# Optimization experiments

Hardware: AMD Instinct MI355X
Metric: run time of the kernel (lower is better)

The kernel has to match this reference:

```python
import jax, jax.numpy as jnp
import numpy as np

B, L, IN_DIM, H, DK, DV = 4, 512, 256, 8, 32, 32
TEMP = DK ** 0.5  # temperature = d_k ** 0.5
LN_EPS = 1e-6


def setup_inputs() -> dict:
    key = jax.random.key(0)
    ks = jax.random.split(key, 5)
    s = 0.05
    return {
        "x": jax.random.normal(ks[0], (B, L, IN_DIM), jnp.float32),
        "w_q": jax.random.normal(ks[1], (IN_DIM, H * DK), jnp.float32) * s,
        "w_k": jax.random.normal(ks[2], (IN_DIM, H * DK), jnp.float32) * s,
        "w_v": jax.random.normal(ks[3], (IN_DIM, H * DV), jnp.float32) * s,
        "w_fc": jax.random.normal(ks[4], (H * DV, IN_DIM), jnp.float32) * s,
        "ln_gamma": jnp.ones((IN_DIM,), jnp.float32),
        "ln_beta": jnp.zeros((IN_DIM,), jnp.float32),
    }


def reference(x, w_q, w_k, w_v, w_fc, ln_gamma, ln_beta):
    # LayerNorm (biased variance, eps inside sqrt, as in torch.nn.LayerNorm)
    mu = jnp.mean(x, axis=-1, keepdims=True)
    var = jnp.var(x, axis=-1, keepdims=True)
    xn = (x - mu) / jnp.sqrt(var + LN_EPS) * ln_gamma + ln_beta
    residual = xn

    # Projections; torch layout after transpose(1,3) is [B, d, H, L]; per-head slice is [B, d, L].
    # We use [B, H, d, L] which yields identical per-head tensors (vectorized over heads).
    q = (xn @ w_q).reshape(B, L, H, DK).transpose(0, 2, 3, 1) / TEMP  # [B,H,DK,L]
    k = (xn @ w_k).reshape(B, L, H, DK).transpose(0, 2, 3, 1)          # [B,H,DK,L]
    v = (xn @ w_v).reshape(B, L, H, DV).transpose(0, 2, 3, 1)          # [B,H,DV,L]

    # L1 distance scores (note the source's index convention):
    # attn[b,h,i,j] = mean_d |q[b,h,d,j] - k[b,h,d,i]|   -> [B,H,L,L]
    attn = jnp.mean(jnp.abs(q[:, :, :, None, :] - k[:, :, :, :, None]), axis=2)
    attn = jax.nn.softmax(attn, axis=-1)

    # out[b,h,d,i] = sum_j v[b,h,d,j] * attn[b,h,i,j]   (torch: bmm(v, attn^T))
    out = jnp.einsum('bhdj,bhij->bhdi', v, attn)  # [B,H,DV,L]
    out = out.reshape(B, H * DV, L).transpose(0, 2, 1)  # head-major concat -> [B,L,H*DV]
    out = out @ w_fc + residual  # use_gamma=False path; dropout is identity at eval

    # extract_attn_map (no_grad in source)
    am = jax.lax.stop_gradient(attn)
    am = jnp.mean(am, axis=1)          # mean over heads -> [B,L,L]
    am = jnp.sum(am, axis=1)           # sum over key axis -> [B,L]
    mn = jnp.min(am, axis=1, keepdims=True)
    mx = jnp.max(am, axis=1, keepdims=True)
    am = (am - mn) / (mx - mn)
    return out, am
```

## Files before the change

kernel.cpp:

```cpp
#include <hip/hip_runtime.h>
#include <hip/hip_fp16.h>
#include <math.h>

#define BATCH 4
#define SEQ   512
#define IND   256
#define NH    8
#define DKV   32
#define BH    32
#define NTOK  2048

__device__ __forceinline__ __half2 habs2_(__half2 x) {
    unsigned u = __builtin_bit_cast(unsigned, x) & 0x7fff7fffu;
    return __builtin_bit_cast(__half2, u);
}
__device__ __forceinline__ __half2 shfl_xor_h2(__half2 x, int m) {
    float f = __builtin_bit_cast(float, x);
    f = __shfl_xor(f, m, 64);
    return __builtin_bit_cast(__half2, f);
}

__global__ void ln_kernel(const float* __restrict__ x,
                          const float* __restrict__ gamma,
                          const float* __restrict__ beta,
                          float* __restrict__ xn,
                          float* __restrict__ am) {
    int row = blockIdx.x;
    int t = threadIdx.x;
    if (blockIdx.x < 8) am[blockIdx.x * 256 + t] = 0.0f;
    float v = x[row * IND + t];
    float s = v, s2 = v * v;
    #pragma unroll
    for (int o = 32; o > 0; o >>= 1) {
        s  += __shfl_xor(s,  o, 64);
        s2 += __shfl_xor(s2, o, 64);
    }
    __shared__ float ls[4], ls2[4];
    int w = t >> 6;
    if ((t & 63) == 0) { ls[w] = s; ls2[w] = s2; }
    __syncthreads();
    s  = ls[0] + ls[1] + ls[2] + ls[3];
    s2 = ls2[0] + ls2[1] + ls2[2] + ls2[3];
    float mu  = s * (1.0f / IND);
    float var = s2 * (1.0f / IND) - mu * mu;
    float r = rsqrtf(var + 1e-6f);
    xn[row * IND + t] = (v - mu) * r * gamma[t] + beta[t];
}

__device__ __forceinline__ void gemm_tile_64(const float* __restrict__ A,
                                             const float* __restrict__ B,
                                             int m0, int n0, int ldb,
                                             float acc[4][4]) {
    __shared__ __align__(16) float As[2][32][68];
    __shared__ __align__(16) float Bs[2][32][68];
    const int t  = threadIdx.x;
    const int tx = t & 15, ty = t >> 4;
    const int am = t >> 3, ac = (t & 7) * 4;
    const int bk = t >> 4, bn = (t & 15) * 4;

    float4 a0, a1, b0, b1;
    auto loadG = [&](int kc) {
        a0 = *(const float4*)&A[(m0 + am) * IND + kc * 32 + ac];
        a1 = *(const float4*)&A[(m0 + 32 + am) * IND + kc * 32 + ac];
        b0 = *(const float4*)&B[(kc * 32 + bk) * ldb + n0 + bn];
        b1 = *(const float4*)&B[(kc * 32 + 16 + bk) * ldb + n0 + bn];
    };
    auto storeL = [&](int buf) {
        As[buf][ac + 0][am] = a0.x; As[buf][ac + 1][am] = a0.y;
        As[buf][ac + 2][am] = a0.z; As[buf][ac + 3][am] = a0.w;
        As[buf][ac + 0][am + 32] = a1.x; As[buf][ac + 1][am + 32] = a1.y;
        As[buf][ac + 2][am + 32] = a1.z; As[buf][ac + 3][am + 32] = a1.w;
        *(float4*)&Bs[buf][bk][bn]      = b0;
        *(float4*)&Bs[buf][16 + bk][bn] = b1;
    };

    loadG(0); storeL(0);
    for (int kc = 0; kc < 8; kc++) {
        __syncthreads();
        if (kc < 7) loadG(kc + 1);
        const int buf = kc & 1;
        #pragma unroll
        for (int kk = 0; kk < 32; kk++) {
            float4 av = *(const float4*)&As[buf][kk][ty * 4];
            float4 bv = *(const float4*)&Bs[buf][kk][tx * 4];
            acc[0][0] = fmaf(av.x, bv.x, acc[0][0]);
            acc[0][1] = fmaf(av.x, bv.y, acc[0][1]);
            acc[0][2] = fmaf(av.x, bv.z, acc[0][2]);
            acc[0][3] = fmaf(av.x, bv.w, acc[0][3]);
            acc[1][0] = fmaf(av.y, bv.x, acc[1][0]);
            acc[1][1] = fmaf(av.y, bv.y, acc[1][1]);
            acc[1][2] = fmaf(av.y, bv.z, acc[1][2]);
            acc[1][3] = fmaf(av.y, bv.w, acc[1][3]);
            acc[2][0] = fmaf(av.z, bv.x, acc[2][0]);
            acc[2][1] = fmaf(av.z, bv.y, acc[2][1]);
            acc[2][2] = fmaf(av.z, bv.z, acc[2][2]);
            acc[2][3] = fmaf(av.z, bv.w, acc[2][3]);
            acc[3][0] = fmaf(av.w, bv.x, acc[3][0]);
            acc[3][1] = fmaf(av.w, bv.y, acc[3][1]);
            acc[3][2] = fmaf(av.w, bv.z, acc[3][2]);
            acc[3][3] = fmaf(av.w, bv.w, acc[3][3]);
        }
        if (kc < 7) { __syncthreads(); storeL((kc + 1) & 1); }
    }
}

__global__ __launch_bounds__(256) void proj_kernel(
        const float* __restrict__ xn,
        const float* __restrict__ wq, const float* __restrict__ wk,
        const float* __restrict__ wv,
        __half* __restrict__ Q, __half* __restrict__ K, __half* __restrict__ V) {
    int which = blockIdx.z;
    const float* W = (which == 0) ? wq : (which == 1) ? wk : wv;
    __half* O = (which == 0) ? Q : (which == 1) ? K : V;
    int m0 = blockIdx.x * 64, n0 = blockIdx.y * 64;
    float acc[4][4] = {};
    gemm_tile_64(xn, W, m0, n0, IND, acc);
    float scale = (which == 0) ? 0.17677669529663687f : 1.0f;
    int tx = threadIdx.x & 15, ty = threadIdx.x >> 4;
    int col = n0 + tx * 4;
    int h = col >> 5, d = col & 31;
    #pragma unroll
    for (int r = 0; r < 4; r++) {
        int tok = m0 + ty * 4 + r;
        int b = tok >> 9, l = tok & 511;
        __half2 p0 = __halves2half2(__float2half_rn(acc[r][0] * scale),
                                    __float2half_rn(acc[r][1] * scale));
        __half2 p1 = __halves2half2(__float2half_rn(acc[r][2] * scale),
                                    __float2half_rn(acc[r][3] * scale));
        __half* dst = O + (((b << 3) + h) * SEQ + l) * DKV + d;
        *(__half2*)dst = p0;
        *(__half2*)(dst + 2) = p1;
    }
}

__global__ __launch_bounds__(256) void attn_kernel(
        const __half* __restrict__ Qh, const __half* __restrict__ Kh,
        const __half* __restrict__ Vh, float* __restrict__ attn_out,
        float* __restrict__ am) {
    __shared__ __align__(16) __half Th[2][128][40];
    const int t = threadIdx.x;
    const int gy = blockIdx.y;
    const int i0 = blockIdx.x * 16;
    const int b = gy >> 3, h = gy & 7;
    const __half* Qb = Qh + gy * SEQ * DKV;
    const __half* Kb = Kh + gy * SEQ * DKV;
    const __half* Vb = Vh + gy * SEQ * DKV;
    const int g = t >> 5, jl = t & 31;
    const int r0 = t >> 2, ch = t & 3;

    __half2 ka[16], kb[16];
    {
        const float4* pa = (const float4*)(Kb + (i0 + g) * DKV);
        const float4* pb = (const float4*)(Kb + (i0 + g + 8) * DKV);
        #pragma unroll
        for (int c = 0; c < 4; c++) {
            float4 va = pa[c], vb = pb[c];
            const __half2* ha = (const __half2*)&va;
            const __half2* hb = (const __half2*)&vb;
            #pragma unroll
            for (int k = 0; k < 4; k++) { ka[c*4+k] = ha[k]; kb[c*4+k] = hb[k]; }
        }
    }

    float vals_a[16], vals_b[16];
    float4 pre0, pre1;

    pre0 = *(const float4*)(Qb + r0 * DKV + ch * 8);
    pre1 = *(const float4*)(Qb + (r0 + 64) * DKV + ch * 8);
    *(float4*)&Th[0][r0][ch * 8] = pre0;
    *(float4*)&Th[0][r0 + 64][ch * 8] = pre1;
    __syncthreads();
    #pragma unroll
    for (int tile = 0; tile < 4; tile++) {
        const int buf = tile & 1;
        if (tile < 3) {
            pre0 = *(const float4*)(Qb + ((tile+1)*128 + r0) * DKV + ch * 8);
            pre1 = *(const float4*)(Qb + ((tile+1)*128 + r0 + 64) * DKV + ch * 8);
        }
        #pragma unroll
        for (int m = 0; m < 4; m++) {
            const int j = jl + m * 32;
            __half2 z = __float2half2_rn(0.0f);
            __half2 sa0 = z, sa1 = z, sb0 = z, sb1 = z;
            #pragma unroll
            for (int c = 0; c < 4; c++) {
                float4 qv = *(const float4*)&Th[buf][j][c * 8];
                const __half2* q2 = (const __half2*)&qv;
                #pragma unroll
                for (int k = 0; k < 4; k++) {
                    __half2 da = habs2_(__hsub2(q2[k], ka[c*4+k]));
                    __half2 db = habs2_(__hsub2(q2[k], kb[c*4+k]));
                    if (k & 1) { sa1 = __hadd2(sa1, da); sb1 = __hadd2(sb1, db); }
                    else       { sa0 = __hadd2(sa0, da); sb0 = __hadd2(sb0, db); }
                }
            }
            __half2 sa = __hadd2(sa0, sa1), sb = __hadd2(sb0, sb1);
            vals_a[tile*4+m] = (__low2float(sa) + __high2float(sa)) * (1.0f/32.0f);
            vals_b[tile*4+m] = (__low2float(sb) + __high2float(sb)) * (1.0f/32.0f);
        }
        if (tile < 3) {
            *(float4*)&Th[buf ^ 1][r0][ch * 8] = pre0;
            *(float4*)&Th[buf ^ 1][r0 + 64][ch * 8] = pre1;
        }
        __syncthreads();
    }

    float mxa = vals_a[0], mxb = vals_b[0];
    #pragma unroll
    for (int m = 1; m < 16; m++) {
        mxa = fmaxf(mxa, vals_a[m]); mxb = fmaxf(mxb, vals_b[m]);
    }
    #pragma unroll
    for (int s = 1; s <= 16; s <<= 1) {
        mxa = fmaxf(mxa, __shfl_xor(mxa, s, 64));
        mxb = fmaxf(mxb, __shfl_xor(mxb, s, 64));
    }
    float sua = 0.0f, sub = 0.0f;
    #pragma unroll
    for (int m = 0; m < 16; m++) {
        vals_a[m] = __expf(vals_a[m] - mxa); sua += vals_a[m];
        vals_b[m] = __expf(vals_b[m] - mxb); sub += vals_b[m];
    }
    #pragma unroll
    for (int s = 1; s <= 16; s <<= 1) {
        sua += __shfl_xor(sua, s, 64);
        sub += __shfl_xor(sub, s, 64);
    }
    float inva = 1.0f / sua, invb = 1.0f / sub;
    #pragma unroll
    for (int m = 0; m < 16; m++) { vals_a[m] *= inva; vals_b[m] *= invb; }

    __half2 acc_a[16], acc_b[16];
    #pragma unroll
    for (int k = 0; k < 16; k++) {
        acc_a[k] = __float2half2_rn(0.0f);
        acc_b[k] = __float2half2_rn(0.0f);
    }
    pre0 = *(const float4*)(Vb + r0 * DKV + ch * 8);
    pre1 = *(const float4*)(Vb + (r0 + 64) * DKV + ch * 8);
    *(float4*)&Th[0][r0][ch * 8] = pre0;
    *(float4*)&Th[0][r0 + 64][ch * 8] = pre1;
    __syncthreads();
    #pragma unroll
    for (int tile = 0; tile < 4; tile++) {
        const int buf = tile & 1;
        if (tile < 3) {
            pre0 = *(const float4*)(Vb + ((tile+1)*128 + r0) * DKV + ch * 8);
            pre1 = *(const float4*)(Vb + ((tile+1)*128 + r0 + 64) * DKV + ch * 8);
        }
        #pragma unroll
        for (int m = 0; m < 4; m++) {
            const int j = jl + m * 32;
            __half2 pa = __float2half2_rn(vals_a[tile*4+m]);
            __half2 pb = __float2half2_rn(vals_b[tile*4+m]);
            #pragma unroll
            for (int c = 0; c < 4; c++) {
                float4 vv = *(const float4*)&Th[buf][j][c * 8];
                const __half2* v2 = (const __half2*)&vv;
                #pragma unroll
                for (int k = 0; k < 4; k++) {
                    acc_a[c*4+k] = __hfma2(pa, v2[k], acc_a[c*4+k]);
                    acc_b[c*4+k] = __hfma2(pb, v2[k], acc_b[c*4+k]);
                }
            }
        }
        if (tile < 3) {
            *(float4*)&Th[buf ^ 1][r0][ch * 8] = pre0;
            *(float4*)&Th[buf ^ 1][r0 + 64][ch * 8] = pre1;
        }
        __syncthreads();
    }

#define REDSTEP(S, C)                                                      \
    {                                                                      \
        _Pragma("unroll")                                                  \
        for (int k = 0; k < (C); k++) {                                    \
            __half2 sa = (jl & (S)) ? acc_a[k] : acc_a[k + (C)];           \
            __half2 sb = (jl & (S)) ? acc_b[k] : acc_b[k + (C)];           \
            __half2 ra = shfl_xor_h2(sa, (S));                             \
            __half2 rb = shfl_xor_h2(sb, (S));                             \
            __half2 qa = (jl & (S)) ? acc_a[k + (C)] : acc_a[k];           \
            __half2 qb = (jl & (S)) ? acc_b[k + (C)] : acc_b[k];           \
            acc_a[k] = __hadd2(qa, ra);                                    \
            acc_b[k] = __hadd2(qb, rb);                                    \
        }                                                                  \
    }
    REDSTEP(16, 8)
    REDSTEP(8, 4)
    REDSTEP(4, 2)
    REDSTEP(2, 1)
#undef REDSTEP
    acc_a[0] = __hadd2(acc_a[0], shfl_xor_h2(acc_a[0], 1));
    acc_b[0] = __hadd2(acc_b[0], shfl_xor_h2(acc_b[0], 1));
    if (!(jl & 1)) {
        int d2 = (jl >> 1) & 15;
        int col = h * 32 + d2 * 2;
        float2 oa = make_float2(__low2float(acc_a[0]), __high2float(acc_a[0]));
        float2 ob = make_float2(__low2float(acc_b[0]), __high2float(acc_b[0]));
        *(float2*)&attn_out[(b * SEQ + i0 + g) * IND + col] = oa;
        *(float2*)&attn_out[(b * SEQ + i0 + g + 8) * IND + col] = ob;
    }

    float colp[16];
    #pragma unroll
    for (int m = 0; m < 16; m++) {
        float cp = vals_a[m] + vals_b[m];
        cp += __shfl_xor(cp, 32, 64);
        colp[m] = cp;
    }
    float* amw = (float*)&Th[0][0][0];
    const int w = t >> 6;
    if (!(t & 32)) {
        #pragma unroll
        for (int m = 0; m < 16; m++) {
            int j = (m >> 2) * 128 + (m & 3) * 32 + jl;
            amw[w * 512 + j] = colp[m];
        }
    }
    __syncthreads();
    #pragma unroll
    for (int n = 0; n < 2; n++) {
        int j = t + n * 256;
        float s = (amw[j] + amw[512 + j] + amw[1024 + j] + amw[1536 + j]) * 0.125f;
        atomicAdd(&am[b * SEQ + j], s);
    }
}

__global__ __launch_bounds__(256) void fc_kernel(
        const float* __restrict__ ao, const float* __restrict__ wfc,
        const float* __restrict__ xn, float* __restrict__ out) {
    int m0 = blockIdx.x * 64, n0 = blockIdx.y * 64;
    float acc[4][4] = {};
    gemm_tile_64(ao, wfc, m0, n0, IND, acc);
    int tx = threadIdx.x & 15, ty = threadIdx.x >> 4;
    #pragma unroll
    for (int r = 0; r < 4; r++) {
        int row = m0 + ty * 4 + r;
        float4 xr = *(const float4*)&xn[row * IND + n0 + tx * 4];
        float4 o = make_float4(acc[r][0] + xr.x, acc[r][1] + xr.y,
                               acc[r][2] + xr.z, acc[r][3] + xr.w);
        *(float4*)&out[row * IND + n0 + tx * 4] = o;
    }
}

__global__ void amnorm_kernel(const float* __restrict__ am,
                              float* __restrict__ out_am) {
    int b = blockIdx.x;
    int t = threadIdx.x;
    float v0 = am[b * SEQ + t];
    float v1 = am[b * SEQ + t + 256];
    float mn = fminf(v0, v1), mx = fmaxf(v0, v1);
    #pragma unroll
    for (int o = 32; o > 0; o >>= 1) {
        mn = fminf(mn, __shfl_xor(mn, o, 64));
        mx = fmaxf(mx, __shfl_xor(mx, o, 64));
    }
    __shared__ float lmn[4], lmx[4];
    int w = t >> 6;
    if ((t & 63) == 0) { lmn[w] = mn; lmx[w] = mx; }
    __syncthreads();
    mn = fminf(fminf(lmn[0], lmn[1]), fminf(lmn[2], lmn[3]));
    mx = fmaxf(fmaxf(lmx[0], lmx[1]), fmaxf(lmx[2], lmx[3]));
    float inv = 1.0f / (mx - mn);
    out_am[b * SEQ + t]       = (v0 - mn) * inv;
    out_am[b * SEQ + t + 256] = (v1 - mn) * inv;
}

extern "C" void kernel_launch(void* const* d_in, const int* in_sizes, int n_in,
                              void* d_out, int out_size, void* d_ws, size_t ws_size,
                              hipStream_t stream) {
    (void)in_sizes; (void)n_in; (void)out_size; (void)ws_size;
    const float* x     = (const float*)d_in[0];
    const float* w_q   = (const float*)d_in[1];
    const float* w_k   = (const float*)d_in[2];
    const float* w_v   = (const float*)d_in[3];
    const float* w_fc  = (const float*)d_in[4];
    const float* gamma = (const float*)d_in[5];
    const float* beta  = (const float*)d_in[6];
    float* out = (float*)d_out;

    float* ws = (float*)d_ws;
    float* xn = ws;
    float* AO = xn + NTOK * IND;
    float* AM = AO + NTOK * IND;
    __half* Qh = (__half*)(AM + NTOK);
    __half* Kh = Qh + BH * SEQ * DKV;
    __half* Vh = Kh + BH * SEQ * DKV;

    hipLaunchKernelGGL(ln_kernel, dim3(NTOK), dim3(256), 0, stream,
                       x, gamma, beta, xn, AM);
    hipLaunchKernelGGL(proj_kernel, dim3(32, 4, 3), dim3(256), 0, stream,
                       xn, w_q, w_k, w_v, Qh, Kh, Vh);
    hipLaunchKernelGGL(attn_kernel, dim3(SEQ / 16, BH), dim3(256), 0, stream,
                       Qh, Kh, Vh, AO, AM);
    hipLaunchKernelGGL(fc_kernel, dim3(32, 4), dim3(256), 0, stream,
                       AO, w_fc, xn, out);
    hipLaunchKernelGGL(amnorm_kernel, dim3(BATCH), dim3(256), 0, stream,
                       AM, out + NTOK * IND);
}
```

Before: 76.71 us.

## Fuse LayerNorm into projection and amnorm into FC, using bf16 MFMA GEMMs

LayerNorm moves into the projection kernel: each block normalizes its 64-row tile in registers and stages it in LDS as bf16. The Q/K/V and FC GEMMs switch from fp32 FMA loops to bf16 MFMA 16x16x32 instructions. The attention-map normalization runs in an extra block column of the FC kernel, so the pipeline drops from five launches to three. In exchange, LayerNorm is recomputed by all 12 column blocks, and bf16 rounding of activations and weights lowers GEMM precision.

```diff
diff --git a/kernel.cpp b/kernel.cpp
--- a/kernel.cpp
+++ b/kernel.cpp
@@ -10,6 +10,16 @@
 #define BH    32
 #define NTOK  2048
 
+typedef __attribute__((ext_vector_type(8))) short short8v;
+typedef __attribute__((ext_vector_type(4))) float floatx4;
+
+__device__ __forceinline__ unsigned f2bf1(float f) {
+    unsigned u = __builtin_bit_cast(unsigned, f);
+    return (u + 0x7fffu + ((u >> 16) & 1u)) >> 16;
+}
+__device__ __forceinline__ unsigned f2bf2(float lo, float hi) {
+    return f2bf1(lo) | (f2bf1(hi) << 16);
+}
 __device__ __forceinline__ __half2 habs2_(__half2 x) {
     unsigned u = __builtin_bit_cast(unsigned, x) & 0x7fff7fffu;
     return __builtin_bit_cast(__half2, u);
@@ -20,117 +30,122 @@
     return __builtin_bit_cast(__half2, f);
 }
 
-__global__ void ln_kernel(const float* __restrict__ x,
-                          const float* __restrict__ gamma,
-                          const float* __restrict__ beta,
-                          float* __restrict__ xn,
-                          float* __restrict__ am) {
-    int row = blockIdx.x;
-    int t = threadIdx.x;
-    if (blockIdx.x < 8) am[blockIdx.x * 256 + t] = 0.0f;
-    float v = x[row * IND + t];
-    float s = v, s2 = v * v;
-    #pragma unroll
-    for (int o = 32; o > 0; o >>= 1) {
-        s  += __shfl_xor(s,  o, 64);
-        s2 += __shfl_xor(s2, o, 64);
-    }
-    __shared__ float ls[4], ls2[4];
-    int w = t >> 6;
-    if ((t & 63) == 0) { ls[w] = s; ls2[w] = s2; }
-    __syncthreads();
-    s  = ls[0] + ls[1] + ls[2] + ls[3];
-    s2 = ls2[0] + ls2[1] + ls2[2] + ls2[3];
-    float mu  = s * (1.0f / IND);
-    float var = s2 * (1.0f / IND) - mu * mu;
-    float r = rsqrtf(var + 1e-6f);
-    xn[row * IND + t] = (v - mu) * r * gamma[t] + beta[t];
-}
-
-__device__ __forceinline__ void gemm_tile_64(const float* __restrict__ A,
-                                             const float* __restrict__ B,
-                                             int m0, int n0, int ldb,
-                                             float acc[4][4]) {
-    __shared__ __align__(16) float As[2][32][68];
-    __shared__ __align__(16) float Bs[2][32][68];
-    const int t  = threadIdx.x;
-    const int tx = t & 15, ty = t >> 4;
-    const int am = t >> 3, ac = (t & 7) * 4;
-    const int bk = t >> 4, bn = (t & 15) * 4;
-
-    float4 a0, a1, b0, b1;
-    auto loadG = [&](int kc) {
-        a0 = *(const float4*)&A[(m0 + am) * IND + kc * 32 + ac];
-        a1 = *(const float4*)&A[(m0 + 32 + am) * IND + kc * 32 + ac];
-        b0 = *(const float4*)&B[(kc * 32 + bk) * ldb + n0 + bn];
-        b1 = *(const float4*)&B[(kc * 32 + 16 + bk) * ldb + n0 + bn];
-    };
-    auto storeL = [&](int buf) {
-        As[buf][ac + 0][am] = a0.x; As[buf][ac + 1][am] = a0.y;
-        As[buf][ac + 2][am] = a0.z; As[buf][ac + 3][am] = a0.w;
-        As[buf][ac + 0][am + 32] = a1.x; As[buf][ac + 1][am + 32] = a1.y;
-        As[buf][ac + 2][am + 32] = a1.z; As[buf][ac + 3][am + 32] = a1.w;
-        *(float4*)&Bs[buf][bk][bn]      = b0;
-        *(float4*)&Bs[buf][16 + bk][bn] = b1;
-    };
-
-    loadG(0); storeL(0);
-    for (int kc = 0; kc < 8; kc++) {
-        __syncthreads();
-        if (kc < 7) loadG(kc + 1);
-        const int buf = kc & 1;
-        #pragma unroll
-        for (int kk = 0; kk < 32; kk++) {
-            float4 av = *(const float4*)&As[buf][kk][ty * 4];
-            float4 bv = *(const float4*)&Bs[buf][kk][tx * 4];
-            acc[0][0] = fmaf(av.x, bv.x, acc[0][0]);
-            acc[0][1] = fmaf(av.x, bv.y, acc[0][1]);
-            acc[0][2] = fmaf(av.x, bv.z, acc[0][2]);
-            acc[0][3] = fmaf(av.x, bv.w, acc[0][3]);
-            acc[1][0] = fmaf(av.y, bv.x, acc[1][0]);
-            acc[1][1] = fmaf(av.y, bv.y, acc[1][1]);
-            acc[1][2] = fmaf(av.y, bv.z, acc[1][2]);
-            acc[1][3] = fmaf(av.y, bv.w, acc[1][3]);
-            acc[2][0] = fmaf(av.z, bv.x, acc[2][0]);
-            acc[2][1] = fmaf(av.z, bv.y, acc[2][1]);
-            acc[2][2] = fmaf(av.z, bv.z, acc[2][2]);
-            acc[2][3] = fmaf(av.z, bv.w, acc[2][3]);
-            acc[3][0] = fmaf(av.w, bv.x, acc[3][0]);
-            acc[3][1] = fmaf(av.w, bv.y, acc[3][1]);
-            acc[3][2] = fmaf(av.w, bv.z, acc[3][2]);
-            acc[3][3] = fmaf(av.w, bv.w, acc[3][3]);
-        }
-        if (kc < 7) { __syncthreads(); storeL((kc + 1) & 1); }
-    }
-}
-
-__global__ __launch_bounds__(256) void proj_kernel(
-        const float* __restrict__ xn,
+__global__ __launch_bounds__(256) void lnproj_kernel(
+        const float* __restrict__ x,
+        const float* __restrict__ gamma, const float* __restrict__ beta,
         const float* __restrict__ wq, const float* __restrict__ wk,
         const float* __restrict__ wv,
+        float* __restrict__ xn, float* __restrict__ am,
         __half* __restrict__ Q, __half* __restrict__ K, __half* __restrict__ V) {
-    int which = blockIdx.z;
+    __shared__ __align__(16) unsigned short As[64][264];
+    __shared__ __align__(16) unsigned short Bs[2][64][40];
+    const int t = threadIdx.x;
+    const int m0 = blockIdx.x * 64;
+    const int y = blockIdx.y;
+    const int which = y >> 2;
+    const int n0 = (y & 3) * 64;
     const float* W = (which == 0) ? wq : (which == 1) ? wk : wv;
     __half* O = (which == 0) ? Q : (which == 1) ? K : V;
-    int m0 = blockIdx.x * 64, n0 = blockIdx.y * 64;
-    float acc[4][4] = {};
-    gemm_tile_64(xn, W, m0, n0, IND, acc);
-    float scale = (which == 0) ? 0.17677669529663687f : 1.0f;
-    int tx = threadIdx.x & 15, ty = threadIdx.x >> 4;
-    int col = n0 + tx * 4;
-    int h = col >> 5, d = col & 31;
-    #pragma unroll
-    for (int r = 0; r < 4; r++) {
-        int tok = m0 + ty * 4 + r;
-        int b = tok >> 9, l = tok & 511;
-        __half2 p0 = __halves2half2(__float2half_rn(acc[r][0] * scale),
-                                    __float2half_rn(acc[r][1] * scale));
-        __half2 p1 = __halves2half2(__float2half_rn(acc[r][2] * scale),
-                                    __float2half_rn(acc[r][3] * scale));
-        __half* dst = O + (((b << 3) + h) * SEQ + l) * DKV + d;
-        *(__half2*)dst = p0;
-        *(__half2*)(dst + 2) = p1;
-    }
+
+    {
+        const int r = t >> 2, q = t & 3;
+        const float* xr = x + (m0 + r) * IND + q * 64;
+        float4 xv[16];
+        float s = 0.0f, s2 = 0.0f;
+        #pragma unroll
+        for (int i = 0; i < 16; i++) {
+            xv[i] = *(const float4*)&xr[i * 4];
+            s  += xv[i].x + xv[i].y + xv[i].z + xv[i].w;
+            s2 += xv[i].x * xv[i].x + xv[i].y * xv[i].y
+                + xv[i].z * xv[i].z + xv[i].w * xv[i].w;
+        }
+        s  += __shfl_xor(s, 1, 64);  s  += __shfl_xor(s, 2, 64);
+        s2 += __shfl_xor(s2, 1, 64); s2 += __shfl_xor(s2, 2, 64);
+        float mu = s * (1.0f / IND);
+        float var = s2 * (1.0f / IND) - mu * mu;
+        float rinv = rsqrtf(var + 1e-6f);
+        const bool dox = (y == 0);
+        if (dox && t < 64) am[m0 + t] = 0.0f;
+        #pragma unroll
+        for (int i = 0; i < 8; i++) {
+            float4 a = xv[2 * i], bv = xv[2 * i + 1];
+            float4 g0 = *(const float4*)&gamma[q * 64 + i * 8];
+            float4 g1 = *(const float4*)&gamma[q * 64 + i * 8 + 4];
+            float4 b0 = *(const float4*)&beta[q * 64 + i * 8];
+            float4 b1 = *(const float4*)&beta[q * 64 + i * 8 + 4];
+            float4 n0v, n1v;
+            n0v.x = (a.x - mu) * rinv * g0.x + b0.x;
+            n0v.y = (a.y - mu) * rinv * g0.y + b0.y;
+            n0v.z = (a.z - mu) * rinv * g0.z + b0.z;
+            n0v.w = (a.w - mu) * rinv * g0.w + b0.w;
+            n1v.x = (bv.x - mu) * rinv * g1.x + b1.x;
+            n1v.y = (bv.y - mu) * rinv * g1.y + b1.y;
+            n1v.z = (bv.z - mu) * rinv * g1.z + b1.z;
+            n1v.w = (bv.w - mu) * rinv * g1.w + b1.w;
+            if (dox) {
+                *(float4*)&xn[(m0 + r) * IND + q * 64 + i * 8] = n0v;
+                *(float4*)&xn[(m0 + r) * IND + q * 64 + i * 8 + 4] = n1v;
+            }
+            uint4 pk;
+            pk.x = f2bf2(n0v.x, n0v.y); pk.y = f2bf2(n0v.z, n0v.w);
+            pk.z = f2bf2(n1v.x, n1v.y); pk.w = f2bf2(n1v.z, n1v.w);
+            *(uint4*)&As[r][q * 64 + i * 8] = pk;
+        }
+    }
+
+    const int w = t >> 6, l = t & 63;
+    const int wm = (w >> 1) * 32, wn = (w & 1) * 32;
+    const int fr = l & 15, fg = l >> 4;
+    floatx4 acc[2][2];
+    #pragma unroll
+    for (int i = 0; i < 2; i++)
+        #pragma unroll
+        for (int j = 0; j < 2; j++) acc[i][j] = (floatx4)(0.0f);
+
+    const int kl = t >> 4, nq = t & 15;
+    auto stageB = [&](int kt, int buf) {
+        float4 b0 = *(const float4*)&W[(kt * 32 + kl) * IND + n0 + nq * 4];
+        float4 b1 = *(const float4*)&W[(kt * 32 + 16 + kl) * IND + n0 + nq * 4];
+        Bs[buf][nq * 4 + 0][kl] = (unsigned short)f2bf1(b0.x);
+        Bs[buf][nq * 4 + 1][kl] = (unsigned short)f2bf1(b0.y);
+        Bs[buf][nq * 4 + 2][kl] = (unsigned short)f2bf1(b0.z);
+        Bs[buf][nq * 4 + 3][kl] = (unsigned short)f2bf1(b0.w);
+        Bs[buf][nq * 4 + 0][kl + 16] = (unsigned short)f2bf1(b1.x);
+        Bs[buf][nq * 4 + 1][kl + 16] = (unsigned short)f2bf1(b1.y);
+        Bs[buf][nq * 4 + 2][kl + 16] = (unsigned short)f2bf1(b1.z);
+        Bs[buf][nq * 4 + 3][kl + 16] = (unsigned short)f2bf1(b1.w);
+    };
+    stageB(0, 0);
+    __syncthreads();
+    #pragma unroll
+    for (int kt = 0; kt < 8; kt++) {
+        if (kt < 7) stageB(kt + 1, (kt + 1) & 1);
+        const int buf = kt & 1;
+        short8v a0 = *(const short8v*)&As[wm + fr][kt * 32 + fg * 8];
+        short8v a1 = *(const short8v*)&As[wm + 16 + fr][kt * 32 + fg * 8];
+        short8v b0 = *(const short8v*)&Bs[buf][wn + fr][fg * 8];
+        short8v b1 = *(const short8v*)&Bs[buf][wn + 16 + fr][fg * 8];
+        acc[0][0] = __builtin_amdgcn_mfma_f32_16x16x32_bf16(a0, b0, acc[0][0], 0, 0, 0);
+        acc[0][1] = __builtin_amdgcn_mfma_f32_16x16x32_bf16(a0, b1, acc[0][1], 0, 0, 0);
+        acc[1][0] = __builtin_amdgcn_mfma_f32_16x16x32_bf16(a1, b0, acc[1][0], 0, 0, 0);
+        acc[1][1] = __builtin_amdgcn_mfma_f32_16x16x32_bf16(a1, b1, acc[1][1], 0, 0, 0);
+        __syncthreads();
+    }
+
+    const float scale = (which == 0) ? 0.17677669529663687f : 1.0f;
+    #pragma unroll
+    for (int mi = 0; mi < 2; mi++)
+        #pragma unroll
+        for (int ni = 0; ni < 2; ni++)
+            #pragma unroll
+            for (int reg = 0; reg < 4; reg++) {
+                int row = m0 + wm + mi * 16 + fg * 4 + reg;
+                int col = n0 + wn + ni * 16 + fr;
+                int b = row >> 9, ll = row & 511;
+                int h = col >> 5, d = col & 31;
+                O[(((b << 3) + h) * SEQ + ll) * DKV + d] =
+                    __float2half_rn(acc[mi][ni][reg] * scale);
+            }
 }
 
 __global__ __launch_bounds__(256) void attn_kernel(
@@ -326,44 +341,102 @@
     }
 }
 
-__global__ __launch_bounds__(256) void fc_kernel(
+__global__ __launch_bounds__(256) void fcam_kernel(
         const float* __restrict__ ao, const float* __restrict__ wfc,
-        const float* __restrict__ xn, float* __restrict__ out) {
-    int m0 = blockIdx.x * 64, n0 = blockIdx.y * 64;
-    float acc[4][4] = {};
-    gemm_tile_64(ao, wfc, m0, n0, IND, acc);
-    int tx = threadIdx.x & 15, ty = threadIdx.x >> 4;
-    #pragma unroll
-    for (int r = 0; r < 4; r++) {
-        int row = m0 + ty * 4 + r;
-        float4 xr = *(const float4*)&xn[row * IND + n0 + tx * 4];
-        float4 o = make_float4(acc[r][0] + xr.x, acc[r][1] + xr.y,
-                               acc[r][2] + xr.z, acc[r][3] + xr.w);
-        *(float4*)&out[row * IND + n0 + tx * 4] = o;
-    }
-}
-
-__global__ void amnorm_kernel(const float* __restrict__ am,
-                              float* __restrict__ out_am) {
-    int b = blockIdx.x;
-    int t = threadIdx.x;
-    float v0 = am[b * SEQ + t];
-    float v1 = am[b * SEQ + t + 256];
-    float mn = fminf(v0, v1), mx = fmaxf(v0, v1);
-    #pragma unroll
-    for (int o = 32; o > 0; o >>= 1) {
-        mn = fminf(mn, __shfl_xor(mn, o, 64));
-        mx = fmaxf(mx, __shfl_xor(mx, o, 64));
-    }
+        const float* __restrict__ xn, const float* __restrict__ am,
+        float* __restrict__ out, float* __restrict__ out_am) {
+    __shared__ __align__(16) unsigned short As[64][264];
+    __shared__ __align__(16) unsigned short Bs[2][64][40];
     __shared__ float lmn[4], lmx[4];
-    int w = t >> 6;
-    if ((t & 63) == 0) { lmn[w] = mn; lmx[w] = mx; }
+    const int t = threadIdx.x;
+
+    if (blockIdx.x == 32) {
+        int b = blockIdx.y;
+        float v0 = am[b * SEQ + t];
+        float v1 = am[b * SEQ + t + 256];
+        float mn = fminf(v0, v1), mx = fmaxf(v0, v1);
+        #pragma unroll
+        for (int o = 32; o > 0; o >>= 1) {
+            mn = fminf(mn, __shfl_xor(mn, o, 64));
+            mx = fmaxf(mx, __shfl_xor(mx, o, 64));
+        }
+        int w = t >> 6;
+        if ((t & 63) == 0) { lmn[w] = mn; lmx[w] = mx; }
+        __syncthreads();
+        mn = fminf(fminf(lmn[0], lmn[1]), fminf(lmn[2], lmn[3]));
+        mx = fmaxf(fmaxf(lmx[0], lmx[1]), fmaxf(lmx[2], lmx[3]));
+        float inv = 1.0f / (mx - mn);
+        out_am[b * SEQ + t]       = (v0 - mn) * inv;
+        out_am[b * SEQ + t + 256] = (v1 - mn) * inv;
+        return;
+    }
+
+    const int m0 = blockIdx.x * 64;
+    const int n0 = blockIdx.y * 64;
+
+    {
+        const int r = t >> 2, q = t & 3;
+        const float* ar = ao + (m0 + r) * IND + q * 64;
+        #pragma unroll
+        for (int i = 0; i < 8; i++) {
+            float4 a = *(const float4*)&ar[i * 8];
+            float4 bv = *(const float4*)&ar[i * 8 + 4];
+            uint4 pk;
+            pk.x = f2bf2(a.x, a.y);  pk.y = f2bf2(a.z, a.w);
+            pk.z = f2bf2(bv.x, bv.y); pk.w = f2bf2(bv.z, bv.w);
+            *(uint4*)&As[r][q * 64 + i * 8] = pk;
+        }
+    }
+
+    const int w = t >> 6, l = t & 63;
+    const int wm = (w >> 1) * 32, wn = (w & 1) * 32;
+    const int fr = l & 15, fg = l >> 4;
+    floatx4 acc[2][2];
+    #pragma unroll
+    for (int i = 0; i < 2; i++)
+        #pragma unroll
+        for (int j = 0; j < 2; j++) acc[i][j] = (floatx4)(0.0f);
+
+    const int kl = t >> 4, nq = t & 15;
+    auto stageB = [&](int kt, int buf) {
+        float4 b0 = *(const float4*)&wfc[(kt * 32 + kl) * IND + n0 + nq * 4];
+        float4 b1 = *(const float4*)&wfc[(kt * 32 + 16 + kl) * IND + n0 + nq * 4];
+        Bs[buf][nq * 4 + 0][kl] = (unsigned short)f2bf1(b0.x);
+        Bs[buf][nq * 4 + 1][kl] = (unsigned short)f2bf1(b0.y);
+        Bs[buf][nq * 4 + 2][kl] = (unsigned short)f2bf1(b0.z);
+        Bs[buf][nq * 4 + 3][kl] = (unsigned short)f2bf1(b0.w);
+        Bs[buf][nq * 4 + 0][kl + 16] = (unsigned short)f2bf1(b1.x);
+        Bs[buf][nq * 4 + 1][kl + 16] = (unsigned short)f2bf1(b1.y);
+        Bs[buf][nq * 4 + 2][kl + 16] = (unsigned short)f2bf1(b1.z);
+        Bs[buf][nq * 4 + 3][kl + 16] = (unsigned short)f2bf1(b1.w);
+    };
+    stageB(0, 0);
     __syncthreads();
-    mn = fminf(fminf(lmn[0], lmn[1]), fminf(lmn[2], lmn[3]));
-    mx = fmaxf(fmaxf(lmx[0], lmx[1]), fmaxf(lmx[2], lmx[3]));
-    float inv = 1.0f / (mx - mn);
-    out_am[b * SEQ + t]       = (v0 - mn) * inv;
-    out_am[b * SEQ + t + 256] = (v1 - mn) * inv;
+    #pragma unroll
+    for (int kt = 0; kt < 8; kt++) {
+        if (kt < 7) stageB(kt + 1, (kt + 1) & 1);
+        const int buf = kt & 1;
+        short8v a0 = *(const short8v*)&As[wm + fr][kt * 32 + fg * 8];
+        short8v a1 = *(const short8v*)&As[wm + 16 + fr][kt * 32 + fg * 8];
+        short8v b0 = *(const short8v*)&Bs[buf][wn + fr][fg * 8];
+        short8v b1 = *(const short8v*)&Bs[buf][wn + 16 + fr][fg * 8];
+        acc[0][0] = __builtin_amdgcn_mfma_f32_16x16x32_bf16(a0, b0, acc[0][0], 0, 0, 0);
+        acc[0][1] = __builtin_amdgcn_mfma_f32_16x16x32_bf16(a0, b1, acc[0][1], 0, 0, 0);
+        acc[1][0] = __builtin_amdgcn_mfma_f32_16x16x32_bf16(a1, b0, acc[1][0], 0, 0, 0);
+        acc[1][1] = __builtin_amdgcn_mfma_f32_16x16x32_bf16(a1, b1, acc[1][1], 0, 0, 0);
+        __syncthreads();
+    }
+
+    #pragma unroll
+    for (int mi = 0; mi < 2; mi++)
+        #pragma unroll
+        for (int ni = 0; ni < 2; ni++)
+            #pragma unroll
+            for (int reg = 0; reg < 4; reg++) {
+                int row = m0 + wm + mi * 16 + fg * 4 + reg;
+                int col = n0 + wn + ni * 16 + fr;
+                out[row * IND + col] = acc[mi][ni][reg] + xn[row * IND + col];
+            }
 }
 
 extern "C" void kernel_launch(void* const* d_in, const int* in_sizes, int n_in,
@@ -387,14 +460,10 @@
     __half* Kh = Qh + BH * SEQ * DKV;
     __half* Vh = Kh + BH * SEQ * DKV;
 
-    hipLaunchKernelGGL(ln_kernel, dim3(NTOK), dim3(256), 0, stream,
-                       x, gamma, beta, xn, AM);
-    hipLaunchKernelGGL(proj_kernel, dim3(32, 4, 3), dim3(256), 0, stream,
-                       xn, w_q, w_k, w_v, Qh, Kh, Vh);
+    hipLaunchKernelGGL(lnproj_kernel, dim3(32, 12), dim3(256), 0, stream,
+                       x, gamma, beta, w_q, w_k, w_v, xn, AM, Qh, Kh, Vh);
     hipLaunchKernelGGL(attn_kernel, dim3(SEQ / 16, BH), dim3(256), 0, stream,
                        Qh, Kh, Vh, AO, AM);
-    hipLaunchKernelGGL(fc_kernel, dim3(32, 4), dim3(256), 0, stream,
-                       AO, w_fc, xn, out);
-    hipLaunchKernelGGL(amnorm_kernel, dim3(BATCH), dim3(256), 0, stream,
-                       AM, out + NTOK * IND);
-}
+    hipLaunchKernelGGL(fcam_kernel, dim3(33, 4), dim3(256), 0, stream,
+                       AO, w_fc, xn, AM, out, out + NTOK * IND);
+}
```

Result: faster. 67.72 us (-11.7%).
